# Kernel tuning notes

Hardware: AMD Instinct MI355X
Metric: run time of the kernel (lower is better)

Reference implementation:

```python
import jax, jax.numpy as jnp
import numpy as np

B = 128          # episodes
L = 512          # static pad length per episode (support or query)
LAMBDA_K_TAU = 0.1


def _masked_cov(x, mask, lengths):
    # x: [B, L, D]; mask: [B, L, 1]; lengths: [B] (float counts)
    x = x * mask
    mean = x.sum(axis=1) / lengths[:, None]                    # [B, D]
    c = (x - mean[:, None, :]) * mask                          # [B, L, D]
    cov = jnp.einsum('bld,ble->bde', c, c)                     # [B, D, D]
    return cov / (lengths - 1.0)[:, None, None]


def _calc_label_cov_inv(task_cov, label_cov):
    d = task_cov.shape[-1]
    eye = jnp.eye(d, dtype=task_cov.dtype)
    m = LAMBDA_K_TAU * label_cov + (1.0 - LAMBDA_K_TAU) * task_cov + 0.1 * eye
    return jnp.linalg.inv(m)


def _separate_qsl(graph_reprs, labels, is_query, batch_index):
    # Re-batch flat [N, D] into padded per-episode support/query tensors.
    N, D = graph_reprs.shape
    g = batch_index * 2 + is_query                             # group id
    perm = jnp.argsort(g)                                      # stable sort
    gs = g[perm]
    first = jnp.searchsorted(gs, gs, side='left')
    rank = jnp.arange(N) - first                               # index within group
    b = batch_index[perm]
    q = is_query[perm]
    row_s = jnp.where(q == 0, rank, L)                         # dummy row L for other kind
    row_q = jnp.where(q == 1, rank, L)
    xp = graph_reprs[perm]
    sup = jnp.zeros((B, L + 1, D), graph_reprs.dtype).at[b, row_s].set(xp)[:, :L]
    qry = jnp.zeros((B, L + 1, D), graph_reprs.dtype).at[b, row_q].set(xp)[:, :L]
    sup_lab = jnp.zeros((B, L + 1), labels.dtype).at[b, row_s].set(labels[perm])[:, :L]
    isq = is_query.astype(jnp.float32)
    sup_len = jnp.zeros((B,), jnp.float32).at[batch_index].add(1.0 - isq)
    qry_len = jnp.zeros((B,), jnp.float32).at[batch_index].add(isq)
    return sup, sup_lab, sup_len, qry, qry_len


def setup_inputs() -> dict:
    key = jax.random.key(0)
    k0, k1, k2, k3 = jax.random.split(key, 4)
    N, D = 49152, 512
    graph_reprs = jax.random.normal(k0, (N, D), jnp.float32)
    labels = jax.random.randint(k1, (N,), 0, 2)
    is_query = jax.random.randint(k2, (N,), 0, 2)
    batch_index = jnp.sort(jax.random.randint(k3, (N,), 0, B))
    log_scale = jnp.full((1,), np.log(1.0 / 16.0), jnp.float32)
    return {"graph_reprs": graph_reprs, "log_scale": log_scale,
            "labels": labels, "is_query": is_query, "batch_index": batch_index}


def reference(graph_reprs, log_scale, labels, is_query, batch_index):
    sup, sup_lab, sup_len, qry, qry_len = _separate_qsl(graph_reprs, labels, is_query, batch_index)
    f = jnp.float32
    support_mask = (jnp.arange(L)[None, :] < sup_len[:, None]).astype(f)[..., None]  # [B,L,1]
    mpos = (sup_lab == 1).astype(f)[..., None] * support_mask
    mneg = (sup_lab == 0).astype(f)[..., None] * support_mask

    pos_mean = (sup * mpos).sum(axis=1) / mpos.sum(axis=1)     # [B, D]
    neg_mean = (sup * mneg).sum(axis=1) / mneg.sum(axis=1)

    task_cov = _masked_cov(sup, support_mask, sup_len)
    pos_cnt = mpos.sum(axis=(1, 2))
    neg_cnt = mneg.sum(axis=(1, 2))
    # Masked covariance == cov of boolean-extracted, re-batched class subsets.
    pos_cov = _masked_cov(sup, mpos, pos_cnt)
    neg_cov = _masked_cov(sup, mneg, neg_cnt)

    pos_inv = _calc_label_cov_inv(task_cov, pos_cov)
    neg_inv = _calc_label_cov_inv(task_cov, neg_cov)

    query_mask = (jnp.arange(L)[None, :] < qry_len[:, None]).astype(f)  # [B, L]
    pos_diff = qry - pos_mean[:, None, :]
    neg_diff = qry - neg_mean[:, None, :]
    # Faithful to original einsum (sums inv over its second index):
    pos_maha = jnp.einsum('bik,bkx,bij->bi', pos_diff, pos_inv, pos_diff) * query_mask
    neg_maha = jnp.einsum('bik,bkx,bij->bi', neg_diff, neg_inv, neg_diff) * query_mask

    logits = jnp.stack([neg_maha, pos_maha], axis=-1)          # [B, L, 2]
    return logits * jnp.exp(log_scale)
```

## Files before the change

### kernel.cpp

```cpp
#include <hip/hip_runtime.h>
#include <cstdint>
#include <cstddef>

#define EPISODES 128
#define LPAD     512
#define DDIM     512
#define NS_CAP   320
#define GTILE    64
#define NPAIRS   15
#define CG_ITERS 14
#define GL_F4    10016
#define KCH      64
#define KSTR     72

typedef __attribute__((ext_vector_type(8))) __bf16 bf16x8;
typedef __attribute__((ext_vector_type(4))) float  floatx4;

__device__ __forceinline__ int lower_bound_dev(const int* __restrict__ a, int n, int key){
    int lo = 0, hi = n;
    while(lo < hi){
        int m = (lo + hi) >> 1;
        if(a[m] < key) lo = m + 1; else hi = m;
    }
    return lo;
}

__device__ __forceinline__ float4 f4add(float4 a, float4 b){
    return make_float4(a.x+b.x, a.y+b.y, a.z+b.z, a.w+b.w);
}
__device__ __forceinline__ float4 f4fma(float s, float4 a, float4 acc){
    return make_float4(acc.x + s*a.x, acc.y + s*a.y, acc.z + s*a.z, acc.w + s*a.w);
}
__device__ __forceinline__ float f4dot(float4 a, float4 b){
    return a.x*b.x + a.y*b.y + a.z*b.z + a.w*b.w;
}
__device__ __forceinline__ float f4sum(float4 a){ return (a.x+a.y)+(a.z+a.w); }

__device__ __forceinline__ unsigned short f2bf(float x){
    unsigned u = __float_as_uint(x);
    u += 0x7FFFu + ((u >> 16) & 1u);
    return (unsigned short)(u >> 16);
}
__device__ __forceinline__ float bf2f(unsigned short h){
    return __uint_as_float(((unsigned)h) << 16);
}

__device__ __forceinline__ float rdlanef(float v, int l){
    return __int_as_float(__builtin_amdgcn_readlane(__float_as_int(v), l));
}
__device__ __forceinline__ float dotb(float4 g, float4 u, int l){
    return g.x*rdlanef(u.x,l) + g.y*rdlanef(u.y,l)
         + g.z*rdlanef(u.z,l) + g.w*rdlanef(u.w,l);
}
__device__ __forceinline__ void gload_lds16(const float4* g, float4* l){
    __builtin_amdgcn_global_load_lds(
        (__attribute__((address_space(1))) void*)g,
        (__attribute__((address_space(3))) void*)l,
        16, 0, 0);
}

__global__ __launch_bounds__(256) void k_prep(
        const int* __restrict__ labels, const int* __restrict__ is_query,
        const int* __restrict__ bidx, const float* __restrict__ X, int N,
        int* __restrict__ sup_idx, int* __restrict__ qry_idx,
        int* __restrict__ sup_lab, int* __restrict__ counts,
        float* __restrict__ task_mean, float* __restrict__ pos_mean,
        float* __restrict__ neg_mean, float* __restrict__ row_sums2)
{
    const int bid  = blockIdx.x;
    const int b    = bid >> 1;
    const int h    = bid & 1;
    const int tid  = threadIdx.x;
    const int lane = tid & 63;
    const int wave = tid >> 6;

    __shared__ int s_start, s_end;
    __shared__ int wq[4];
    __shared__ int s_runq, s_npos;
    __shared__ int   sidx[NS_CAP];
    __shared__ float slabf[NS_CAP];
    __shared__ float4 pa[4][64];
    __shared__ float4 pp[4][64];

    if(tid == 0){
        s_start = lower_bound_dev(bidx, N, b);
        s_end   = lower_bound_dev(bidx, N, b + 1);
        s_runq  = 0;
        s_npos  = 0;
    }
    __syncthreads();
    const int start = s_start, end = s_end;

    for(int base = start; base < end; base += 256){
        int idx   = base + tid;
        bool valid = idx < end;
        int q   = valid ? is_query[idx] : 0;
        int lab = valid ? labels[idx]   : 0;
        unsigned long long m = __ballot(q == 1);
        if(lane == 0) wq[wave] = __popcll(m);
        __syncthreads();
        int woff = 0;
        for(int w = 0; w < wave; w++) woff += wq[w];
        int qbefore = __popcll(m & ((1ull << lane) - 1ull)) + woff;
        int runq0 = s_runq;
        int chunk_total = wq[0] + wq[1] + wq[2] + wq[3];
        if(valid){
            int pos_in_seg = idx - start;
            if(q){
                int qr = runq0 + qbefore;
                if(h == 0 && qr < LPAD) qry_idx[b * LPAD + qr] = idx;
            } else {
                int sr = pos_in_seg - runq0 - qbefore;
                if(sr < LPAD){
                    if(h == 0){
                        sup_idx[b * LPAD + sr] = idx;
                        sup_lab[b * LPAD + sr] = lab;
                    }
                    if(sr < NS_CAP){ sidx[sr] = idx; slabf[sr] = (float)lab; }
                    if(lab == 1) atomicAdd(&s_npos, 1);
                }
            }
        }
        __syncthreads();
        if(tid == 0) s_runq = runq0 + chunk_total;
        __syncthreads();
    }

    const int nq   = s_runq;
    const int ns   = (end - start) - nq;
    const int npos = s_npos;
    const int nneg = ns - npos;
    if(h == 0 && tid == 0){
        counts[b*4 + 0] = ns;
        counts[b*4 + 1] = nq;
        counts[b*4 + 2] = npos;
        counts[b*4 + 3] = nneg;
    }
    const int nsb = min(ns, NS_CAP);

    const float4* X4 = (const float4*)X;
    const int colg = h*64 + lane;
    float4 sa = make_float4(0.f,0.f,0.f,0.f);
    float4 sp = make_float4(0.f,0.f,0.f,0.f);
    int r = wave;
    for(; r + 12 < nsb; r += 16){
        int n0 = sidx[r], n1 = sidx[r+4], n2 = sidx[r+8], n3 = sidx[r+12];
        float l0 = slabf[r], l1 = slabf[r+4], l2 = slabf[r+8], l3 = slabf[r+12];
        float4 x0 = X4[(size_t)n0*128 + colg];
        float4 x1 = X4[(size_t)n1*128 + colg];
        float4 x2 = X4[(size_t)n2*128 + colg];
        float4 x3 = X4[(size_t)n3*128 + colg];
        sa = f4add(sa, f4add(f4add(x0,x1), f4add(x2,x3)));
        sp = f4fma(l0,x0, f4fma(l1,x1, f4fma(l2,x2, f4fma(l3,x3, sp))));
        float r0s = f4sum(x0), r1s = f4sum(x1), r2s = f4sum(x2), r3s = f4sum(x3);
        #pragma unroll
        for(int off = 32; off; off >>= 1){
            r0s += __shfl_xor(r0s, off); r1s += __shfl_xor(r1s, off);
            r2s += __shfl_xor(r2s, off); r3s += __shfl_xor(r3s, off);
        }
        if(lane == 0){
            row_sums2[(b*LPAD + r   )*2 + h] = r0s;
            row_sums2[(b*LPAD + r+4 )*2 + h] = r1s;
            row_sums2[(b*LPAD + r+8 )*2 + h] = r2s;
            row_sums2[(b*LPAD + r+12)*2 + h] = r3s;
        }
    }
    for(; r < nsb; r += 4){
        int n = sidx[r];
        float l = slabf[r];
        float4 x = X4[(size_t)n*128 + colg];
        sa = f4add(sa, x);
        sp = f4fma(l, x, sp);
        float rs = f4sum(x);
        #pragma unroll
        for(int off = 32; off; off >>= 1) rs += __shfl_xor(rs, off);
        if(lane == 0) row_sums2[(b*LPAD + r)*2 + h] = rs;
    }
    pa[wave][lane] = sa;
    pp[wave][lane] = sp;
    __syncthreads();
    if(tid < 64){
        float4 A = f4add(f4add(pa[0][tid],pa[1][tid]), f4add(pa[2][tid],pa[3][tid]));
        float4 P = f4add(f4add(pp[0][tid],pp[1][tid]), f4add(pp[2][tid],pp[3][tid]));
        float4 Nn = make_float4(A.x-P.x, A.y-P.y, A.z-P.z, A.w-P.w);
        float ia = 1.f/(float)ns, ip = 1.f/(float)npos, in = 1.f/(float)nneg;
        int c = b*128 + h*64 + tid;
        ((float4*)task_mean)[c] = make_float4(A.x*ia, A.y*ia, A.z*ia, A.w*ia);
        ((float4*)pos_mean )[c] = make_float4(P.x*ip, P.y*ip, P.z*ip, P.w*ip);
        ((float4*)neg_mean )[c] = make_float4(Nn.x*in, Nn.y*in, Nn.z*in, Nn.w*in);
    }
}

__global__ __launch_bounds__(256) void k_gram(
        const float* __restrict__ X, const int* __restrict__ sup_idx,
        const int* __restrict__ counts, float* __restrict__ G0)
{
    const int bid = blockIdx.x;
    const int b   = bid / NPAIRS;
    int tp = bid % NPAIRS;
    int ti = 0;
    while((ti+1)*(ti+2)/2 <= tp) ti++;
    const int tj  = tp - ti*(ti+1)/2;
    const int tid = threadIdx.x;
    const int lane = tid & 63;
    const int wave = tid >> 6;

    const int ns  = counts[b*4 + 0];
    const int nsc = min(ns, NS_CAP);
    if(ti * GTILE >= nsc) return;
    const bool diag = (ti == tj);

    __shared__ int ia[GTILE], ib[GTILE];
    __shared__ __align__(16) unsigned short SM[4 * GTILE * KSTR];
    unsigned short* SAh = SM;
    unsigned short* SAl = SM + GTILE*KSTR;
    unsigned short* SBh = SM + 2*GTILE*KSTR;
    unsigned short* SBl = SM + 3*GTILE*KSTR;

    if(tid < GTILE)        ia[tid]    = sup_idx[b*LPAD + min(ti*GTILE + tid,      nsc-1)];
    else if(tid < 2*GTILE) ib[tid-64] = sup_idx[b*LPAD + min(tj*GTILE + (tid-64), nsc-1)];

    const unsigned short* Bh = diag ? SAh : SBh;
    const unsigned short* Bl = diag ? SAl : SBl;

    const int ry = (wave >> 1) * 32;
    const int cx = (wave & 1) * 32;
    const int fr = lane & 15;
    const int fq = (lane >> 4) * 8;

    floatx4 acc[2][2];
    acc[0][0] = (floatx4){0.f,0.f,0.f,0.f};
    acc[0][1] = (floatx4){0.f,0.f,0.f,0.f};
    acc[1][0] = (floatx4){0.f,0.f,0.f,0.f};
    acc[1][1] = (floatx4){0.f,0.f,0.f,0.f};

    for(int k0 = 0; k0 < DDIM; k0 += KCH){
        __syncthreads();
        #pragma unroll
        for(int p = 0; p < 4; p++){
            int e = tid + p*256;
            int row = e >> 4, kq = e & 15;
            float4 xa = *(const float4*)(X + (size_t)ia[row]*DDIM + k0 + kq*4);
            ushort4 hh, ll;
            hh.x = f2bf(xa.x); ll.x = f2bf(xa.x - bf2f(hh.x));
            hh.y = f2bf(xa.y); ll.y = f2bf(xa.y - bf2f(hh.y));
            hh.z = f2bf(xa.z); ll.z = f2bf(xa.z - bf2f(hh.z));
            hh.w = f2bf(xa.w); ll.w = f2bf(xa.w - bf2f(hh.w));
            *(ushort4*)&SAh[row*KSTR + kq*4] = hh;
            *(ushort4*)&SAl[row*KSTR + kq*4] = ll;
            if(!diag){
                float4 xb = *(const float4*)(X + (size_t)ib[row]*DDIM + k0 + kq*4);
                ushort4 h2, l2;
                h2.x = f2bf(xb.x); l2.x = f2bf(xb.x - bf2f(h2.x));
                h2.y = f2bf(xb.y); l2.y = f2bf(xb.y - bf2f(h2.y));
                h2.z = f2bf(xb.z); l2.z = f2bf(xb.z - bf2f(h2.z));
                h2.w = f2bf(xb.w); l2.w = f2bf(xb.w - bf2f(h2.w));
                *(ushort4*)&SBh[row*KSTR + kq*4] = h2;
                *(ushort4*)&SBl[row*KSTR + kq*4] = l2;
            }
        }
        __syncthreads();
        #pragma unroll
        for(int ks = 0; ks < KCH; ks += 32){
            bf16x8 ah0 = *(const bf16x8*)&SAh[(ry     + fr)*KSTR + ks + fq];
            bf16x8 ah1 = *(const bf16x8*)&SAh[(ry + 16 + fr)*KSTR + ks + fq];
            bf16x8 al0 = *(const bf16x8*)&SAl[(ry     + fr)*KSTR + ks + fq];
            bf16x8 al1 = *(const bf16x8*)&SAl[(ry + 16 + fr)*KSTR + ks + fq];
            bf16x8 bh0 = *(const bf16x8*)&Bh[(cx     + fr)*KSTR + ks + fq];
            bf16x8 bh1 = *(const bf16x8*)&Bh[(cx + 16 + fr)*KSTR + ks + fq];
            bf16x8 bl0 = *(const bf16x8*)&Bl[(cx     + fr)*KSTR + ks + fq];
            bf16x8 bl1 = *(const bf16x8*)&Bl[(cx + 16 + fr)*KSTR + ks + fq];
            acc[0][0] = __builtin_amdgcn_mfma_f32_16x16x32_bf16(ah0, bh0, acc[0][0], 0,0,0);
            acc[0][1] = __builtin_amdgcn_mfma_f32_16x16x32_bf16(ah0, bh1, acc[0][1], 0,0,0);
            acc[1][0] = __builtin_amdgcn_mfma_f32_16x16x32_bf16(ah1, bh0, acc[1][0], 0,0,0);
            acc[1][1] = __builtin_amdgcn_mfma_f32_16x16x32_bf16(ah1, bh1, acc[1][1], 0,0,0);
            acc[0][0] = __builtin_amdgcn_mfma_f32_16x16x32_bf16(ah0, bl0, acc[0][0], 0,0,0);
            acc[0][1] = __builtin_amdgcn_mfma_f32_16x16x32_bf16(ah0, bl1, acc[0][1], 0,0,0);
            acc[1][0] = __builtin_amdgcn_mfma_f32_16x16x32_bf16(ah1, bl0, acc[1][0], 0,0,0);
            acc[1][1] = __builtin_amdgcn_mfma_f32_16x16x32_bf16(ah1, bl1, acc[1][1], 0,0,0);
            acc[0][0] = __builtin_amdgcn_mfma_f32_16x16x32_bf16(al0, bh0, acc[0][0], 0,0,0);
            acc[0][1] = __builtin_amdgcn_mfma_f32_16x16x32_bf16(al0, bh1, acc[0][1], 0,0,0);
            acc[1][0] = __builtin_amdgcn_mfma_f32_16x16x32_bf16(al1, bh0, acc[1][0], 0,0,0);
            acc[1][1] = __builtin_amdgcn_mfma_f32_16x16x32_bf16(al1, bh1, acc[1][1], 0,0,0);
        }
    }

    float4* Gf4 = (float4*)(G0 + (size_t)b * NS_CAP * NS_CAP);
    const int q = lane >> 4, j = lane & 15;
    #pragma unroll
    for(int sy = 0; sy < 2; sy++)
        #pragma unroll
        for(int sx = 0; sx < 2; sx++){
            int cq = ((ti*GTILE + ry + sy*16) >> 2) + q;
            int t  = tj*GTILE + cx + sx*16 + j;
            Gf4[(size_t)cq * NS_CAP + t] =
                make_float4(acc[sy][sx].x, acc[sy][sx].y, acc[sy][sx].z, acc[sy][sx].w);
        }

    if(!diag){
        __syncthreads();
        float* Tb = (float*)SM;
        #pragma unroll
        for(int sy = 0; sy < 2; sy++)
            #pragma unroll
            for(int sx = 0; sx < 2; sx++){
                int r0 = ry + sy*16 + 4*q;
                int c  = cx + sx*16 + j;
                Tb[(r0+0)*68 + c] = acc[sy][sx].x;
                Tb[(r0+1)*68 + c] = acc[sy][sx].y;
                Tb[(r0+2)*68 + c] = acc[sy][sx].z;
                Tb[(r0+3)*68 + c] = acc[sy][sx].w;
            }
        __syncthreads();
        for(int e = tid; e < 16*GTILE; e += 256){
            int cc = e >> 6;
            int r  = e & 63;
            float4 v = *(const float4*)&Tb[r*68 + 4*cc];
            Gf4[(size_t)(tj*16 + cc) * NS_CAP + ti*GTILE + r] = v;
        }
    }
}

extern __shared__ float4 gl4[];

__global__ __launch_bounds__(512, 2) void k_cgc(
        const float* __restrict__ X, const float* __restrict__ G0,
        const int* __restrict__ sup_idx, const int* __restrict__ sup_lab,
        const int* __restrict__ counts, const float* __restrict__ row_sums2,
        float* __restrict__ vout)
{
    const int bid  = blockIdx.x;
    const int sys  = ((bid & 7) << 5) | (bid >> 3);
    const int b    = sys >> 1;
    const int cls  = sys & 1;
    const int tid  = threadIdx.x;
    const int lane = tid & 63;
    const int wave = tid >> 6;

    __shared__ __align__(16) float u[NS_CAP];
    __shared__ int   idx_l[NS_CAP];
    __shared__ float P[64];

    const int ns   = counts[b*4 + 0];
    const int nsc  = min(ns, NS_CAP);
    const int ncls = cls ? counts[b*4 + 2] : counts[b*4 + 3];
    const float c_task = 0.9f / (float)(ns - 1);
    const float c_cls  = 0.1f / (float)(ncls - 1);
    const float inv_ns = 1.f / (float)ns;
    const float inv_nc = 1.f / (float)ncls;
    const float4* G4 = (const float4*)(G0 + (size_t)b * NS_CAP * NS_CAP);
    const float4* u4 = (const float4*)u;
    const int nf4 = (nsc + 3) >> 2;
    const int c4l = min(nf4, GL_F4 / nsc);

    const bool mth = tid < NS_CAP;
    const bool own = tid < nsc;
    float mfl = 0.f, sraw = 0.f;
    if(own){
        mfl  = (sup_lab[b*LPAD + tid] == cls) ? 1.f : 0.f;
        float2 rs = ((const float2*)row_sums2)[b*LPAD + tid];
        sraw = rs.x + rs.y;
    }
    for(int s = tid; s < nsc; s += 512) idx_l[s] = sup_idx[b*LPAD + s];
    if(tid < 64) P[tid] = 0.f;

    {
        const int nchunk = (nsc + 63) >> 6;
        for(int ch = 0; ch < nchunk; ch++){
            const int t = (ch << 6) + lane;
            const bool act = t < nsc;
            const float4* gsrc = G4 + t;
            float4*       ldst = gl4 + t;
            for(int c4 = wave; c4 < c4l; c4 += 8){
                if(act) gload_lds16(gsrc + (size_t)c4 * NS_CAP, ldst + c4 * nsc);
            }
        }
    }
    __syncthreads();

    auto bundle = [&](float v0, float v1, float v2, float v3, float v4,
                      float* S){
        #pragma unroll
        for(int off = 32; off; off >>= 1){
            v0 += __shfl_xor(v0, off); v1 += __shfl_xor(v1, off);
            v2 += __shfl_xor(v2, off); v3 += __shfl_xor(v3, off);
            v4 += __shfl_xor(v4, off);
        }
        if(lane == 0){
            P[wave*8 + 0] = v0; P[wave*8 + 1] = v1; P[wave*8 + 2] = v2;
            P[wave*8 + 3] = v3; P[wave*8 + 4] = v4;
        }
        __syncthreads();
        float pv = P[lane];
        pv += __shfl_xor(pv, 8);
        pv += __shfl_xor(pv, 16);
        pv += __shfl_xor(pv, 32);
        S[0] = __shfl(pv, 0); S[1] = __shfl(pv, 1); S[2] = __shfl(pv, 2);
        S[3] = __shfl(pv, 3); S[4] = __shfl(pv, 4);
    };

    const bool fastu = (nf4 <= 64);

    auto matvec = [&]() -> float {
        float s0 = 0.f, s1 = 0.f, s2 = 0.f, s3 = 0.f;
        if(fastu){
            if((wave << 6) < nsc){
                float4 ubc = u4[lane < nf4 ? lane : 0];
                asm volatile("" : "+v"(ubc.x), "+v"(ubc.y), "+v"(ubc.z), "+v"(ubc.w));
                const int row = own ? tid : (nsc - 1);
                const float4* gq = gl4 + row;
                int c4 = 0;
                for(; c4 + 8 <= c4l; c4 += 8){
                    float4 g0 = gq[(c4+0)*nsc], g1 = gq[(c4+1)*nsc];
                    float4 g2 = gq[(c4+2)*nsc], g3 = gq[(c4+3)*nsc];
                    float4 g4_ = gq[(c4+4)*nsc], g5 = gq[(c4+5)*nsc];
                    float4 g6 = gq[(c4+6)*nsc], g7 = gq[(c4+7)*nsc];
                    s0 += dotb(g0, ubc, c4+0); s1 += dotb(g1, ubc, c4+1);
                    s2 += dotb(g2, ubc, c4+2); s3 += dotb(g3, ubc, c4+3);
                    s0 += dotb(g4_, ubc, c4+4); s1 += dotb(g5, ubc, c4+5);
                    s2 += dotb(g6, ubc, c4+6); s3 += dotb(g7, ubc, c4+7);
                }
                for(; c4 < c4l; c4++) s0 += dotb(gq[c4*nsc], ubc, c4);
                for(; c4 + 4 <= nf4; c4 += 4){
                    float4 h0 = G4[(size_t)(c4+0)*NS_CAP + row];
                    float4 h1 = G4[(size_t)(c4+1)*NS_CAP + row];
                    float4 h2 = G4[(size_t)(c4+2)*NS_CAP + row];
                    float4 h3 = G4[(size_t)(c4+3)*NS_CAP + row];
                    s0 += dotb(h0, ubc, c4+0); s1 += dotb(h1, ubc, c4+1);
                    s2 += dotb(h2, ubc, c4+2); s3 += dotb(h3, ubc, c4+3);
                }
                for(; c4 < nf4; c4++)
                    s0 += dotb(G4[(size_t)c4*NS_CAP + row], ubc, c4);
            }
        } else {
            if(own){
                const float4* gq = gl4 + tid;
                int c4 = 0;
                for(; c4 + 8 <= c4l; c4 += 8){
                    float4 g0 = gq[(c4+0)*nsc], g1 = gq[(c4+1)*nsc];
                    float4 g2 = gq[(c4+2)*nsc], g3 = gq[(c4+3)*nsc];
                    float4 g4_ = gq[(c4+4)*nsc], g5 = gq[(c4+5)*nsc];
                    float4 g6 = gq[(c4+6)*nsc], g7 = gq[(c4+7)*nsc];
                    s0 += f4dot(g0, u4[c4+0]); s1 += f4dot(g1, u4[c4+1]);
                    s2 += f4dot(g2, u4[c4+2]); s3 += f4dot(g3, u4[c4+3]);
                    s0 += f4dot(g4_, u4[c4+4]); s1 += f4dot(g5, u4[c4+5]);
                    s2 += f4dot(g6, u4[c4+6]); s3 += f4dot(g7, u4[c4+7]);
                }
                for(; c4 < c4l; c4++) s0 += f4dot(gq[c4*nsc], u4[c4]);
                for(; c4 + 8 <= nf4; c4 += 8){
                    float4 g[8];
                    #pragma unroll
                    for(int jj = 0; jj < 8; jj++) g[jj] = G4[(size_t)(c4+jj)*NS_CAP + tid];
                    #pragma unroll
                    for(int jj = 0; jj < 8; jj++){
                        float d = f4dot(g[jj], u4[c4+jj]);
                        if((jj & 3) == 0) s0 += d; else if((jj & 3) == 1) s1 += d;
                        else if((jj & 3) == 2) s2 += d; else s3 += d;
                    }
                }
                for(; c4 < nf4; c4++) s0 += f4dot(G4[(size_t)c4*NS_CAP + tid], u4[c4]);
            }
        }
        float t = (s0 + s1) + (s2 + s3);
        return own ? t : 0.f;
    };

    float S[5];
    bundle(sraw, mfl * sraw, 0.f, 0.f, 0.f, S);
    float A0 = S[0] * inv_ns, A1 = S[1] * inv_nc;
    float cr = own ? -10.f * (c_task*(sraw - A0) + mfl*c_cls*(sraw - A1)) : 0.f;
    if(mth) u[tid] = cr;
    __syncthreads();
    float tr = matvec();

    float cp = 0.f, cq = 0.f, tq = 0.f, cx = 0.f;
    float gamma_old = 1.f, alpha_old = 1.f;
    bool first = true;

    for(int it = 0; it < CG_ITERS; ++it){
        bundle(tr, mfl*tr, tr*tr, mfl*tr*tr, tr*cr, S);
        A0 = S[0] * inv_ns; A1 = S[1] * inv_nc;
        float gamma = S[4];
        float delta = 0.1f*gamma + c_task*(S[2] - S[0]*A0)
                                 + c_cls *(S[3] - S[1]*A1);
        float beta  = first ? 0.f : gamma / gamma_old;
        float denom = first ? delta : (delta - beta * gamma / alpha_old);
        float alpha = (gamma < 1e-30f) ? 0.f : gamma / denom;
        float ur = own ? (c_task*(tr - A0) + mfl*c_cls*(tr - A1)) : 0.f;
        float cw = 0.1f*cr + ur;
        cp = cr + beta * cp;
        cq = cw + beta * cq;
        cx += alpha * cp;
        if(it == CG_ITERS - 1 || gamma < 1e-26f) break;
        if(mth) u[tid] = ur;
        __syncthreads();
        float gv = matvec();
        float tw = 0.1f*tr + gv;
        tq = tw + beta * tq;
        cr -= alpha * cq;
        tr -= alpha * tq;
        gamma_old = gamma; alpha_old = alpha; first = false;
    }

    __syncthreads();
    if(mth) u[tid] = own ? cx : 0.f;
    __syncthreads();
    const float4* X4 = (const float4*)X;
    const int f4c = tid & 127;
    const int rg  = tid >> 7;
    float4 acc = make_float4(0.f,0.f,0.f,0.f);
    int s = rg;
    for(; s + 28 < nsc; s += 32){
        int n0 = idx_l[s],    n1 = idx_l[s+4],  n2 = idx_l[s+8],  n3 = idx_l[s+12];
        int n4 = idx_l[s+16], n5 = idx_l[s+20], n6 = idx_l[s+24], n7 = idx_l[s+28];
        float w0 = u[s],    w1 = u[s+4],  w2 = u[s+8],  w3 = u[s+12];
        float w4 = u[s+16], w5 = u[s+20], w6 = u[s+24], w7 = u[s+28];
        float4 x0 = X4[(size_t)n0*128 + f4c];
        float4 x1 = X4[(size_t)n1*128 + f4c];
        float4 x2 = X4[(size_t)n2*128 + f4c];
        float4 x3 = X4[(size_t)n3*128 + f4c];
        float4 x4 = X4[(size_t)n4*128 + f4c];
        float4 x5 = X4[(size_t)n5*128 + f4c];
        float4 x6 = X4[(size_t)n6*128 + f4c];
        float4 x7 = X4[(size_t)n7*128 + f4c];
        acc = f4fma(w0,x0, f4fma(w1,x1, f4fma(w2,x2, f4fma(w3,x3, acc))));
        acc = f4fma(w4,x4, f4fma(w5,x5, f4fma(w6,x6, f4fma(w7,x7, acc))));
    }
    for(; s < nsc; s += 4)
        acc = f4fma(u[s], X4[(size_t)idx_l[s]*128 + f4c], acc);
    gl4[rg*128 + f4c] = acc;
    __syncthreads();
    if(tid < 128){
        float4 v = f4add(f4add(gl4[tid], gl4[128+tid]),
                         f4add(gl4[256+tid], gl4[384+tid]));
        v.x += 10.f; v.y += 10.f; v.z += 10.f; v.w += 10.f;
        ((float4*)vout)[(size_t)sys * 128 + tid] = v;
    }
}

__global__ __launch_bounds__(256) void k_out(
        const float* __restrict__ X,
        const int* __restrict__ qry_idx, const int* __restrict__ counts,
        const float* __restrict__ pos_mean, const float* __restrict__ neg_mean,
        const float* __restrict__ vsol, const float* __restrict__ log_scale,
        float* __restrict__ out)
{
    const int bid  = blockIdx.x;
    const int b    = bid >> 1;
    const int h    = bid & 1;
    const int tid  = threadIdx.x;
    const int lane = tid & 63;
    const int wave = tid >> 6;

    __shared__ __align__(16) float vpos[DDIM];
    __shared__ __align__(16) float vneg[DDIM];
    __shared__ float red4[4][4];
    __shared__ float sc[4];

    const int nq  = counts[b*4 + 1];
    const int nqc = min(nq, LPAD);
    const float scale = expf(log_scale[0]);

    float pm0 = pos_mean[b*DDIM + tid], pm1 = pos_mean[b*DDIM + tid + 256];
    float nm0 = neg_mean[b*DDIM + tid], nm1 = neg_mean[b*DDIM + tid + 256];
    float vp0 = vsol[(size_t)(b*2 + 1) * DDIM + tid];
    float vp1 = vsol[(size_t)(b*2 + 1) * DDIM + tid + 256];
    float vn0 = vsol[(size_t)(b*2 + 0) * DDIM + tid];
    float vn1 = vsol[(size_t)(b*2 + 0) * DDIM + tid + 256];
    vpos[tid] = vp0; vpos[tid + 256] = vp1;
    vneg[tid] = vn0; vneg[tid + 256] = vn1;

    float smp = pm0 + pm1;
    float smn = nm0 + nm1;
    float mvp = pm0 * vp0 + pm1 * vp1;
    float mvn = nm0 * vn0 + nm1 * vn1;
    #pragma unroll
    for(int off = 32; off; off >>= 1){
        smp += __shfl_xor(smp, off);
        smn += __shfl_xor(smn, off);
        mvp += __shfl_xor(mvp, off);
        mvn += __shfl_xor(mvn, off);
    }
    if(lane == 0){
        red4[wave][0] = smp; red4[wave][1] = smn;
        red4[wave][2] = mvp; red4[wave][3] = mvn;
    }
    __syncthreads();
    if(tid < 4) sc[tid] = red4[0][tid] + red4[1][tid] + red4[2][tid] + red4[3][tid];
    __syncthreads();

    const float4* vp4 = (const float4*)vpos;
    const float4* vn4 = (const float4*)vneg;
    const float4 vpa = vp4[lane], vpb = vp4[lane + 64];
    const float4 vna = vn4[lane], vnb = vn4[lane + 64];
    for(int r = wave + 4*h; r < nqc; r += 16){
        int r2 = r + 8;
        bool has2 = r2 < nqc;
        int n  = qry_idx[b * LPAD + r];
        int n2 = qry_idx[b * LPAD + (has2 ? r2 : r)];
        const float4* xr = (const float4*)(X + (size_t)n  * DDIM);
        const float4* yr = (const float4*)(X + (size_t)n2 * DDIM);
        float4 x0 = xr[lane], x1 = xr[lane + 64];
        float4 y0 = yr[lane], y1 = yr[lane + 64];
        float tp = f4dot(x0, vpa) + f4dot(x1, vpb);
        float tn = f4dot(x0, vna) + f4dot(x1, vnb);
        float sx = f4sum(x0) + f4sum(x1);
        float tp2 = f4dot(y0, vpa) + f4dot(y1, vpb);
        float tn2 = f4dot(y0, vna) + f4dot(y1, vnb);
        float sx2 = f4sum(y0) + f4sum(y1);
        #pragma unroll
        for(int off = 32; off; off >>= 1){
            tp  += __shfl_xor(tp,  off);
            tn  += __shfl_xor(tn,  off);
            sx  += __shfl_xor(sx,  off);
            tp2 += __shfl_xor(tp2, off);
            tn2 += __shfl_xor(tn2, off);
            sx2 += __shfl_xor(sx2, off);
        }
        if(lane == 0){
            float mp = (tp - sc[2]) * (sx - sc[0]);
            float mn = (tn - sc[3]) * (sx - sc[1]);
            ((float2*)out)[(size_t)b * LPAD + r] = make_float2(mn * scale, mp * scale);
            if(has2){
                float mp2 = (tp2 - sc[2]) * (sx2 - sc[0]);
                float mn2 = (tn2 - sc[3]) * (sx2 - sc[1]);
                ((float2*)out)[(size_t)b * LPAD + r2] = make_float2(mn2 * scale, mp2 * scale);
            }
        }
    }
    const int lo = max(nqc, h * 256), hi = (h + 1) * 256;
    for(int r = lo + tid; r < hi; r += 256)
        ((float2*)out)[(size_t)b * LPAD + r] = make_float2(0.f, 0.f);
}

extern "C" void kernel_launch(void* const* d_in, const int* in_sizes, int n_in,
                              void* d_out, int out_size, void* d_ws, size_t ws_size,
                              hipStream_t stream)
{
    const float* X         = (const float*)d_in[0];
    const float* log_scale = (const float*)d_in[1];
    const int*   labels    = (const int*)d_in[2];
    const int*   is_query  = (const int*)d_in[3];
    const int*   bidx      = (const int*)d_in[4];
    const int N = in_sizes[2];

    char* ws = (char*)d_ws;
    auto alloc = [&](size_t bytes) -> char* {
        char* p = ws;
        ws += (bytes + 255) & ~(size_t)255;
        return p;
    };
    int*   sup_idx   = (int*)  alloc((size_t)EPISODES * LPAD * sizeof(int));
    int*   qry_idx   = (int*)  alloc((size_t)EPISODES * LPAD * sizeof(int));
    int*   sup_lab   = (int*)  alloc((size_t)EPISODES * LPAD * sizeof(int));
    int*   counts    = (int*)  alloc((size_t)EPISODES * 4 * sizeof(int));
    float* task_mean = (float*)alloc((size_t)EPISODES * DDIM * sizeof(float));
    float* pos_mean  = (float*)alloc((size_t)EPISODES * DDIM * sizeof(float));
    float* neg_mean  = (float*)alloc((size_t)EPISODES * DDIM * sizeof(float));
    float* vsol      = (float*)alloc((size_t)EPISODES * 2 * DDIM * sizeof(float));
    float* row_sums2 = (float*)alloc((size_t)EPISODES * LPAD * 2 * sizeof(float));
    float* G0        = (float*)alloc((size_t)EPISODES * NS_CAP * NS_CAP * sizeof(float));
    (void)ws_size;
    (void)task_mean;

    k_prep<<<EPISODES*2, 256, 0, stream>>>(labels, is_query, bidx, X, N,
                                           sup_idx, qry_idx, sup_lab, counts,
                                           task_mean, pos_mean, neg_mean, row_sums2);
    k_gram<<<EPISODES * NPAIRS, 256, 0, stream>>>(X, sup_idx, counts, G0);
    k_cgc<<<EPISODES * 2, 512, GL_F4 * sizeof(float4), stream>>>(
                                            X, G0, sup_idx, sup_lab, counts,
                                            row_sums2, vsol);
    k_out<<<EPISODES*2, 256, 0, stream>>>(X, qry_idx, counts, pos_mean, neg_mean,
                                          vsol, log_scale, (float*)d_out);
}
```

Baseline: 307.2 us.

## Enlarge Gram tiles to 96 and split CG matvec columns across two thread halves

The Gram kernel now uses 96x96 tiles with a 3x3 MFMA fragment grid per wave, cutting the number of tile pairs from 15 to 10 and reusing each loaded fragment more often. Because tiles no longer divide the 320 cap evenly, stores are bounds-guarded. In the CG kernel the fast matvec path splits the column range between the two 256-thread halves and combines the partial sums through shared memory with an extra barrier. The shared-memory budget is shrunk slightly to fit the exchange buffer. The costs are higher register pressure from nine accumulators, wasted work on partial edge tiles, and one more sync per matvec.

```diff
diff --git a/kernel.cpp b/kernel.cpp
--- a/kernel.cpp
+++ b/kernel.cpp
@@ -6,10 +6,10 @@
 #define LPAD     512
 #define DDIM     512
 #define NS_CAP   320
-#define GTILE    64
-#define NPAIRS   15
+#define GTILE    96
+#define NPAIRS   10
 #define CG_ITERS 14
-#define GL_F4    10016
+#define GL_F4    9984
 #define KCH      64
 #define KSTR     72
 
@@ -217,27 +217,28 @@
     unsigned short* SBh = SM + 2*GTILE*KSTR;
     unsigned short* SBl = SM + 3*GTILE*KSTR;
 
-    if(tid < GTILE)        ia[tid]    = sup_idx[b*LPAD + min(ti*GTILE + tid,      nsc-1)];
-    else if(tid < 2*GTILE) ib[tid-64] = sup_idx[b*LPAD + min(tj*GTILE + (tid-64), nsc-1)];
+    if(tid < GTILE)        ia[tid]     = sup_idx[b*LPAD + min(ti*GTILE + tid,       nsc-1)];
+    else if(tid < 2*GTILE) ib[tid-96]  = sup_idx[b*LPAD + min(tj*GTILE + (tid-96),  nsc-1)];
 
     const unsigned short* Bh = diag ? SAh : SBh;
     const unsigned short* Bl = diag ? SAl : SBl;
 
-    const int ry = (wave >> 1) * 32;
-    const int cx = (wave & 1) * 32;
+    const int ry = (wave >> 1) * 48;
+    const int cx = (wave & 1) * 48;
     const int fr = lane & 15;
     const int fq = (lane >> 4) * 8;
 
-    floatx4 acc[2][2];
-    acc[0][0] = (floatx4){0.f,0.f,0.f,0.f};
-    acc[0][1] = (floatx4){0.f,0.f,0.f,0.f};
-    acc[1][0] = (floatx4){0.f,0.f,0.f,0.f};
-    acc[1][1] = (floatx4){0.f,0.f,0.f,0.f};
+    floatx4 acc[3][3];
+    #pragma unroll
+    for(int m = 0; m < 3; m++)
+        #pragma unroll
+        for(int n = 0; n < 3; n++)
+            acc[m][n] = (floatx4){0.f,0.f,0.f,0.f};
 
     for(int k0 = 0; k0 < DDIM; k0 += KCH){
         __syncthreads();
         #pragma unroll
-        for(int p = 0; p < 4; p++){
+        for(int p = 0; p < 6; p++){
             int e = tid + p*256;
             int row = e >> 4, kq = e & 15;
             float4 xa = *(const float4*)(X + (size_t)ia[row]*DDIM + k0 + kq*4);
@@ -262,61 +263,62 @@
         __syncthreads();
         #pragma unroll
         for(int ks = 0; ks < KCH; ks += 32){
-            bf16x8 ah0 = *(const bf16x8*)&SAh[(ry     + fr)*KSTR + ks + fq];
-            bf16x8 ah1 = *(const bf16x8*)&SAh[(ry + 16 + fr)*KSTR + ks + fq];
-            bf16x8 al0 = *(const bf16x8*)&SAl[(ry     + fr)*KSTR + ks + fq];
-            bf16x8 al1 = *(const bf16x8*)&SAl[(ry + 16 + fr)*KSTR + ks + fq];
-            bf16x8 bh0 = *(const bf16x8*)&Bh[(cx     + fr)*KSTR + ks + fq];
-            bf16x8 bh1 = *(const bf16x8*)&Bh[(cx + 16 + fr)*KSTR + ks + fq];
-            bf16x8 bl0 = *(const bf16x8*)&Bl[(cx     + fr)*KSTR + ks + fq];
-            bf16x8 bl1 = *(const bf16x8*)&Bl[(cx + 16 + fr)*KSTR + ks + fq];
-            acc[0][0] = __builtin_amdgcn_mfma_f32_16x16x32_bf16(ah0, bh0, acc[0][0], 0,0,0);
-            acc[0][1] = __builtin_amdgcn_mfma_f32_16x16x32_bf16(ah0, bh1, acc[0][1], 0,0,0);
-            acc[1][0] = __builtin_amdgcn_mfma_f32_16x16x32_bf16(ah1, bh0, acc[1][0], 0,0,0);
-            acc[1][1] = __builtin_amdgcn_mfma_f32_16x16x32_bf16(ah1, bh1, acc[1][1], 0,0,0);
-            acc[0][0] = __builtin_amdgcn_mfma_f32_16x16x32_bf16(ah0, bl0, acc[0][0], 0,0,0);
-            acc[0][1] = __builtin_amdgcn_mfma_f32_16x16x32_bf16(ah0, bl1, acc[0][1], 0,0,0);
-            acc[1][0] = __builtin_amdgcn_mfma_f32_16x16x32_bf16(ah1, bl0, acc[1][0], 0,0,0);
-            acc[1][1] = __builtin_amdgcn_mfma_f32_16x16x32_bf16(ah1, bl1, acc[1][1], 0,0,0);
-            acc[0][0] = __builtin_amdgcn_mfma_f32_16x16x32_bf16(al0, bh0, acc[0][0], 0,0,0);
-            acc[0][1] = __builtin_amdgcn_mfma_f32_16x16x32_bf16(al0, bh1, acc[0][1], 0,0,0);
-            acc[1][0] = __builtin_amdgcn_mfma_f32_16x16x32_bf16(al1, bh0, acc[1][0], 0,0,0);
-            acc[1][1] = __builtin_amdgcn_mfma_f32_16x16x32_bf16(al1, bh1, acc[1][1], 0,0,0);
+            bf16x8 ah[3], al[3], bh[3], bl[3];
+            #pragma unroll
+            for(int m = 0; m < 3; m++){
+                ah[m] = *(const bf16x8*)&SAh[(ry + 16*m + fr)*KSTR + ks + fq];
+                al[m] = *(const bf16x8*)&SAl[(ry + 16*m + fr)*KSTR + ks + fq];
+                bh[m] = *(const bf16x8*)&Bh [(cx + 16*m + fr)*KSTR + ks + fq];
+                bl[m] = *(const bf16x8*)&Bl [(cx + 16*m + fr)*KSTR + ks + fq];
+            }
+            #pragma unroll
+            for(int m = 0; m < 3; m++)
+                #pragma unroll
+                for(int n = 0; n < 3; n++){
+                    acc[m][n] = __builtin_amdgcn_mfma_f32_16x16x32_bf16(ah[m], bh[n], acc[m][n], 0,0,0);
+                    acc[m][n] = __builtin_amdgcn_mfma_f32_16x16x32_bf16(ah[m], bl[n], acc[m][n], 0,0,0);
+                    acc[m][n] = __builtin_amdgcn_mfma_f32_16x16x32_bf16(al[m], bh[n], acc[m][n], 0,0,0);
+                }
         }
     }
 
     float4* Gf4 = (float4*)(G0 + (size_t)b * NS_CAP * NS_CAP);
     const int q = lane >> 4, j = lane & 15;
     #pragma unroll
-    for(int sy = 0; sy < 2; sy++)
-        #pragma unroll
-        for(int sx = 0; sx < 2; sx++){
+    for(int sy = 0; sy < 3; sy++)
+        #pragma unroll
+        for(int sx = 0; sx < 3; sx++){
             int cq = ((ti*GTILE + ry + sy*16) >> 2) + q;
             int t  = tj*GTILE + cx + sx*16 + j;
-            Gf4[(size_t)cq * NS_CAP + t] =
-                make_float4(acc[sy][sx].x, acc[sy][sx].y, acc[sy][sx].z, acc[sy][sx].w);
+            if(cq < (NS_CAP >> 2) && t < NS_CAP)
+                Gf4[(size_t)cq * NS_CAP + t] =
+                    make_float4(acc[sy][sx].x, acc[sy][sx].y, acc[sy][sx].z, acc[sy][sx].w);
         }
 
     if(!diag){
         __syncthreads();
         float* Tb = (float*)SM;
         #pragma unroll
-        for(int sy = 0; sy < 2; sy++)
+        for(int sy = 0; sy < 3; sy++)
             #pragma unroll
-            for(int sx = 0; sx < 2; sx++){
+            for(int sx = 0; sx < 3; sx++){
                 int r0 = ry + sy*16 + 4*q;
                 int c  = cx + sx*16 + j;
-                Tb[(r0+0)*68 + c] = acc[sy][sx].x;
-                Tb[(r0+1)*68 + c] = acc[sy][sx].y;
-                Tb[(r0+2)*68 + c] = acc[sy][sx].z;
-                Tb[(r0+3)*68 + c] = acc[sy][sx].w;
-            }
-        __syncthreads();
-        for(int e = tid; e < 16*GTILE; e += 256){
-            int cc = e >> 6;
-            int r  = e & 63;
-            float4 v = *(const float4*)&Tb[r*68 + 4*cc];
-            Gf4[(size_t)(tj*16 + cc) * NS_CAP + ti*GTILE + r] = v;
+                Tb[(r0+0)*100 + c] = acc[sy][sx].x;
+                Tb[(r0+1)*100 + c] = acc[sy][sx].y;
+                Tb[(r0+2)*100 + c] = acc[sy][sx].z;
+                Tb[(r0+3)*100 + c] = acc[sy][sx].w;
+            }
+        __syncthreads();
+        for(int e = tid; e < 24*GTILE; e += 256){
+            int cc = e / GTILE;
+            int r  = e - cc*GTILE;
+            int gq2 = tj*24 + cc;
+            int t2  = ti*GTILE + r;
+            if(gq2 < (NS_CAP >> 2) && t2 < NS_CAP){
+                float4 v = *(const float4*)&Tb[r*100 + 4*cc];
+                Gf4[(size_t)gq2 * NS_CAP + t2] = v;
+            }
         }
     }
 }
@@ -336,10 +338,13 @@
     const int tid  = threadIdx.x;
     const int lane = tid & 63;
     const int wave = tid >> 6;
+    const int half = tid >> 8;
+    const int hrow = tid & 255;
 
     __shared__ __align__(16) float u[NS_CAP];
     __shared__ int   idx_l[NS_CAP];
     __shared__ float P[64];
+    __shared__ float exch[256];
 
     const int ns   = counts[b*4 + 0];
     const int nsc  = min(ns, NS_CAP);
@@ -352,6 +357,7 @@
     const float4* u4 = (const float4*)u;
     const int nf4 = (nsc + 3) >> 2;
     const int c4l = min(nf4, GL_F4 / nsc);
+    const int c4m = min(nf4, ((nf4 >> 1) + 3) & ~3);
 
     const bool mth = tid < NS_CAP;
     const bool own = tid < nsc;
@@ -402,15 +408,20 @@
     const bool fastu = (nf4 <= 64);
 
     auto matvec = [&]() -> float {
-        float s0 = 0.f, s1 = 0.f, s2 = 0.f, s3 = 0.f;
         if(fastu){
-            if((wave << 6) < nsc){
+            float p = 0.f;
+            if(((wave & 3) << 6) < nsc){
                 float4 ubc = u4[lane < nf4 ? lane : 0];
                 asm volatile("" : "+v"(ubc.x), "+v"(ubc.y), "+v"(ubc.z), "+v"(ubc.w));
-                const int row = own ? tid : (nsc - 1);
+                const bool ownr = hrow < nsc;
+                const int row = ownr ? hrow : (nsc - 1);
                 const float4* gq = gl4 + row;
-                int c4 = 0;
-                for(; c4 + 8 <= c4l; c4 += 8){
+                float s0 = 0.f, s1 = 0.f, s2 = 0.f, s3 = 0.f;
+                const int lo = half ? c4m : 0;
+                const int hi = half ? nf4 : c4m;
+                const int lim = min(hi, c4l);
+                int c4 = lo;
+                for(; c4 + 8 <= lim; c4 += 8){
                     float4 g0 = gq[(c4+0)*nsc], g1 = gq[(c4+1)*nsc];
                     float4 g2 = gq[(c4+2)*nsc], g3 = gq[(c4+3)*nsc];
                     float4 g4_ = gq[(c4+4)*nsc], g5 = gq[(c4+5)*nsc];
@@ -420,8 +431,8 @@
                     s0 += dotb(g4_, ubc, c4+4); s1 += dotb(g5, ubc, c4+5);
                     s2 += dotb(g6, ubc, c4+6); s3 += dotb(g7, ubc, c4+7);
                 }
-                for(; c4 < c4l; c4++) s0 += dotb(gq[c4*nsc], ubc, c4);
-                for(; c4 + 4 <= nf4; c4 += 4){
+                for(; c4 < lim; c4++) s0 += dotb(gq[c4*nsc], ubc, c4);
+                for(; c4 + 4 <= hi; c4 += 4){
                     float4 h0 = G4[(size_t)(c4+0)*NS_CAP + row];
                     float4 h1 = G4[(size_t)(c4+1)*NS_CAP + row];
                     float4 h2 = G4[(size_t)(c4+2)*NS_CAP + row];
@@ -429,10 +440,16 @@
                     s0 += dotb(h0, ubc, c4+0); s1 += dotb(h1, ubc, c4+1);
                     s2 += dotb(h2, ubc, c4+2); s3 += dotb(h3, ubc, c4+3);
                 }
-                for(; c4 < nf4; c4++)
+                for(; c4 < hi; c4++)
                     s0 += dotb(G4[(size_t)c4*NS_CAP + row], ubc, c4);
-            }
+                p = ownr ? ((s0 + s1) + (s2 + s3)) : 0.f;
+            }
+            if(half) exch[hrow] = p;
+            __syncthreads();
+            float t = (half == 0 && own) ? (p + exch[hrow]) : 0.f;
+            return t;
         } else {
+            float s0 = 0.f, s1 = 0.f, s2 = 0.f, s3 = 0.f;
             if(own){
                 const float4* gq = gl4 + tid;
                 int c4 = 0;
@@ -460,9 +477,9 @@
                 }
                 for(; c4 < nf4; c4++) s0 += f4dot(G4[(size_t)c4*NS_CAP + tid], u4[c4]);
             }
-        }
-        float t = (s0 + s1) + (s2 + s3);
-        return own ? t : 0.f;
+            float t = (s0 + s1) + (s2 + s3);
+            return own ? t : 0.f;
+        }
     };
 
     float S[5];
```

Measured after the change: 340.7 us. 10.9% more time.

## Precompute bf16 hi/lo support rows in prep and split CG matvec across halves

Applied to the files above, without the earlier changes.

k_prep now writes split bf16 hi/lo copies of the gathered support rows into a packed per-episode workspace, zero-padded to a 64-row boundary. k_gram then loads these tiles straight into XOR-swizzled LDS with global_load_lds, so it no longer does gathered fp32 loads and per-tile conversion repeated across tile pairs. In k_cgc's fast matvec path, both 256-thread halves of the block now take half of the columns each and combine partial sums through shared memory, with a slight LDS budget cut. The cost is extra global writes and workspace for the bf16 copy, plus an added barrier in every matvec.

```diff
diff --git a/kernel.cpp b/kernel.cpp
--- a/kernel.cpp
+++ b/kernel.cpp
@@ -9,9 +9,9 @@
 #define GTILE    64
 #define NPAIRS   15
 #define CG_ITERS 14
-#define GL_F4    10016
+#define GL_F4    9984
 #define KCH      64
-#define KSTR     72
+#define XBF_ROW  1024
 
 typedef __attribute__((ext_vector_type(8))) __bf16 bf16x8;
 typedef __attribute__((ext_vector_type(4))) float  floatx4;
@@ -44,6 +44,12 @@
 __device__ __forceinline__ float bf2f(unsigned short h){
     return __uint_as_float(((unsigned)h) << 16);
 }
+__device__ __forceinline__ void cvt_hilo(float4 x, ushort4& hh, ushort4& ll){
+    hh.x = f2bf(x.x); ll.x = f2bf(x.x - bf2f(hh.x));
+    hh.y = f2bf(x.y); ll.y = f2bf(x.y - bf2f(hh.y));
+    hh.z = f2bf(x.z); ll.z = f2bf(x.z - bf2f(hh.z));
+    hh.w = f2bf(x.w); ll.w = f2bf(x.w - bf2f(hh.w));
+}
 
 __device__ __forceinline__ float rdlanef(float v, int l){
     return __int_as_float(__builtin_amdgcn_readlane(__float_as_int(v), l));
@@ -52,9 +58,9 @@
     return g.x*rdlanef(u.x,l) + g.y*rdlanef(u.y,l)
          + g.z*rdlanef(u.z,l) + g.w*rdlanef(u.w,l);
 }
-__device__ __forceinline__ void gload_lds16(const float4* g, float4* l){
+__device__ __forceinline__ void gload_lds16(const void* g, void* l){
     __builtin_amdgcn_global_load_lds(
-        (__attribute__((address_space(1))) void*)g,
+        (const __attribute__((address_space(1))) void*)g,
         (__attribute__((address_space(3))) void*)l,
         16, 0, 0);
 }
@@ -65,7 +71,8 @@
         int* __restrict__ sup_idx, int* __restrict__ qry_idx,
         int* __restrict__ sup_lab, int* __restrict__ counts,
         float* __restrict__ task_mean, float* __restrict__ pos_mean,
-        float* __restrict__ neg_mean, float* __restrict__ row_sums2)
+        float* __restrict__ neg_mean, float* __restrict__ row_sums2,
+        unsigned short* __restrict__ Xbf)
 {
     const int bid  = blockIdx.x;
     const int b    = bid >> 1;
@@ -152,6 +159,22 @@
         float4 x3 = X4[(size_t)n3*128 + colg];
         sa = f4add(sa, f4add(f4add(x0,x1), f4add(x2,x3)));
         sp = f4fma(l0,x0, f4fma(l1,x1, f4fma(l2,x2, f4fma(l3,x3, sp))));
+        {
+            ushort4 hh, ll;
+            size_t rb;
+            rb = ((size_t)(b*NS_CAP + r   ) << 10);
+            cvt_hilo(x0, hh, ll);
+            *(ushort4*)&Xbf[rb + colg*4] = hh;  *(ushort4*)&Xbf[rb + 512 + colg*4] = ll;
+            rb = ((size_t)(b*NS_CAP + r+4 ) << 10);
+            cvt_hilo(x1, hh, ll);
+            *(ushort4*)&Xbf[rb + colg*4] = hh;  *(ushort4*)&Xbf[rb + 512 + colg*4] = ll;
+            rb = ((size_t)(b*NS_CAP + r+8 ) << 10);
+            cvt_hilo(x2, hh, ll);
+            *(ushort4*)&Xbf[rb + colg*4] = hh;  *(ushort4*)&Xbf[rb + 512 + colg*4] = ll;
+            rb = ((size_t)(b*NS_CAP + r+12) << 10);
+            cvt_hilo(x3, hh, ll);
+            *(ushort4*)&Xbf[rb + colg*4] = hh;  *(ushort4*)&Xbf[rb + 512 + colg*4] = ll;
+        }
         float r0s = f4sum(x0), r1s = f4sum(x1), r2s = f4sum(x2), r3s = f4sum(x3);
         #pragma unroll
         for(int off = 32; off; off >>= 1){
@@ -171,10 +194,25 @@
         float4 x = X4[(size_t)n*128 + colg];
         sa = f4add(sa, x);
         sp = f4fma(l, x, sp);
+        {
+            ushort4 hh, ll;
+            size_t rb = ((size_t)(b*NS_CAP + r) << 10);
+            cvt_hilo(x, hh, ll);
+            *(ushort4*)&Xbf[rb + colg*4] = hh;  *(ushort4*)&Xbf[rb + 512 + colg*4] = ll;
+        }
         float rs = f4sum(x);
         #pragma unroll
         for(int off = 32; off; off >>= 1) rs += __shfl_xor(rs, off);
         if(lane == 0) row_sums2[(b*LPAD + r)*2 + h] = rs;
+    }
+    {
+        const int padf = min((nsb + 63) & ~63, NS_CAP);
+        ushort4 z; z.x = z.y = z.z = z.w = 0;
+        for(int rz = nsb + wave; rz < padf; rz += 4){
+            size_t rb = ((size_t)(b*NS_CAP + rz) << 10);
+            *(ushort4*)&Xbf[rb + colg*4] = z;
+            *(ushort4*)&Xbf[rb + 512 + colg*4] = z;
+        }
     }
     pa[wave][lane] = sa;
     pp[wave][lane] = sp;
@@ -192,7 +230,7 @@
 }
 
 __global__ __launch_bounds__(256) void k_gram(
-        const float* __restrict__ X, const int* __restrict__ sup_idx,
+        const unsigned short* __restrict__ Xbf,
         const int* __restrict__ counts, float* __restrict__ G0)
 {
     const int bid = blockIdx.x;
@@ -210,23 +248,18 @@
     if(ti * GTILE >= nsc) return;
     const bool diag = (ti == tj);
 
-    __shared__ int ia[GTILE], ib[GTILE];
-    __shared__ __align__(16) unsigned short SM[4 * GTILE * KSTR];
-    unsigned short* SAh = SM;
-    unsigned short* SAl = SM + GTILE*KSTR;
-    unsigned short* SBh = SM + 2*GTILE*KSTR;
-    unsigned short* SBl = SM + 3*GTILE*KSTR;
-
-    if(tid < GTILE)        ia[tid]    = sup_idx[b*LPAD + min(ti*GTILE + tid,      nsc-1)];
-    else if(tid < 2*GTILE) ib[tid-64] = sup_idx[b*LPAD + min(tj*GTILE + (tid-64), nsc-1)];
-
-    const unsigned short* Bh = diag ? SAh : SBh;
-    const unsigned short* Bl = diag ? SAl : SBl;
-
+    __shared__ __align__(16) unsigned short SM[4 * GTILE * 64];
+    unsigned short* const SAh = SM;
+    unsigned short* const SAl = SM + 4096;
+    const unsigned short* Bh = diag ? SAh : (SM + 8192);
+    const unsigned short* Bl = diag ? SAl : (SM + 12288);
+
+    const int r8  = lane >> 3;
+    const int blk = lane & 7;
+    const int fr = lane & 15;
+    const int fq = (lane >> 4) * 8;
     const int ry = (wave >> 1) * 32;
     const int cx = (wave & 1) * 32;
-    const int fr = lane & 15;
-    const int fq = (lane >> 4) * 8;
 
     floatx4 acc[2][2];
     acc[0][0] = (floatx4){0.f,0.f,0.f,0.f};
@@ -234,42 +267,44 @@
     acc[1][0] = (floatx4){0.f,0.f,0.f,0.f};
     acc[1][1] = (floatx4){0.f,0.f,0.f,0.f};
 
+    const int xr = blk ^ r8;
     for(int k0 = 0; k0 < DDIM; k0 += KCH){
         __syncthreads();
         #pragma unroll
-        for(int p = 0; p < 4; p++){
-            int e = tid + p*256;
-            int row = e >> 4, kq = e & 15;
-            float4 xa = *(const float4*)(X + (size_t)ia[row]*DDIM + k0 + kq*4);
-            ushort4 hh, ll;
-            hh.x = f2bf(xa.x); ll.x = f2bf(xa.x - bf2f(hh.x));
-            hh.y = f2bf(xa.y); ll.y = f2bf(xa.y - bf2f(hh.y));
-            hh.z = f2bf(xa.z); ll.z = f2bf(xa.z - bf2f(hh.z));
-            hh.w = f2bf(xa.w); ll.w = f2bf(xa.w - bf2f(hh.w));
-            *(ushort4*)&SAh[row*KSTR + kq*4] = hh;
-            *(ushort4*)&SAl[row*KSTR + kq*4] = ll;
-            if(!diag){
-                float4 xb = *(const float4*)(X + (size_t)ib[row]*DDIM + k0 + kq*4);
-                ushort4 h2, l2;
-                h2.x = f2bf(xb.x); l2.x = f2bf(xb.x - bf2f(h2.x));
-                h2.y = f2bf(xb.y); l2.y = f2bf(xb.y - bf2f(h2.y));
-                h2.z = f2bf(xb.z); l2.z = f2bf(xb.z - bf2f(h2.z));
-                h2.w = f2bf(xb.w); l2.w = f2bf(xb.w - bf2f(h2.w));
-                *(ushort4*)&SBh[row*KSTR + kq*4] = h2;
-                *(ushort4*)&SBl[row*KSTR + kq*4] = l2;
+        for(int i = 0; i < 4; i++){
+            int e  = wave*4 + i;
+            int pl = e >> 3, g = e & 7;
+            int row = g*8 + r8;
+            const unsigned short* src = Xbf
+                + ((size_t)(b*NS_CAP + ti*GTILE + row) << 10)
+                + pl*512 + k0 + (xr << 3);
+            gload_lds16(src, SM + pl*4096 + row*64 + blk*8);
+        }
+        if(!diag){
+            #pragma unroll
+            for(int i = 0; i < 4; i++){
+                int e  = wave*4 + i;
+                int pl = e >> 3, g = e & 7;
+                int row = g*8 + r8;
+                const unsigned short* src = Xbf
+                    + ((size_t)(b*NS_CAP + tj*GTILE + row) << 10)
+                    + pl*512 + k0 + (xr << 3);
+                gload_lds16(src, SM + 8192 + pl*4096 + row*64 + blk*8);
             }
         }
         __syncthreads();
         #pragma unroll
         for(int ks = 0; ks < KCH; ks += 32){
-            bf16x8 ah0 = *(const bf16x8*)&SAh[(ry     + fr)*KSTR + ks + fq];
-            bf16x8 ah1 = *(const bf16x8*)&SAh[(ry + 16 + fr)*KSTR + ks + fq];
-            bf16x8 al0 = *(const bf16x8*)&SAl[(ry     + fr)*KSTR + ks + fq];
-            bf16x8 al1 = *(const bf16x8*)&SAl[(ry + 16 + fr)*KSTR + ks + fq];
-            bf16x8 bh0 = *(const bf16x8*)&Bh[(cx     + fr)*KSTR + ks + fq];
-            bf16x8 bh1 = *(const bf16x8*)&Bh[(cx + 16 + fr)*KSTR + ks + fq];
-            bf16x8 bl0 = *(const bf16x8*)&Bl[(cx     + fr)*KSTR + ks + fq];
-            bf16x8 bl1 = *(const bf16x8*)&Bl[(cx + 16 + fr)*KSTR + ks + fq];
+            const int j  = (ks + fq) >> 3;
+            const int jx = (j ^ (fr & 7)) << 3;
+            bf16x8 ah0 = *(const bf16x8*)&SAh[(ry      + fr)*64 + jx];
+            bf16x8 ah1 = *(const bf16x8*)&SAh[(ry + 16 + fr)*64 + jx];
+            bf16x8 al0 = *(const bf16x8*)&SAl[(ry      + fr)*64 + jx];
+            bf16x8 al1 = *(const bf16x8*)&SAl[(ry + 16 + fr)*64 + jx];
+            bf16x8 bh0 = *(const bf16x8*)&Bh [(cx      + fr)*64 + jx];
+            bf16x8 bh1 = *(const bf16x8*)&Bh [(cx + 16 + fr)*64 + jx];
+            bf16x8 bl0 = *(const bf16x8*)&Bl [(cx      + fr)*64 + jx];
+            bf16x8 bl1 = *(const bf16x8*)&Bl [(cx + 16 + fr)*64 + jx];
             acc[0][0] = __builtin_amdgcn_mfma_f32_16x16x32_bf16(ah0, bh0, acc[0][0], 0,0,0);
             acc[0][1] = __builtin_amdgcn_mfma_f32_16x16x32_bf16(ah0, bh1, acc[0][1], 0,0,0);
             acc[1][0] = __builtin_amdgcn_mfma_f32_16x16x32_bf16(ah1, bh0, acc[1][0], 0,0,0);
@@ -336,10 +371,13 @@
     const int tid  = threadIdx.x;
     const int lane = tid & 63;
     const int wave = tid >> 6;
+    const int half = tid >> 8;
+    const int hrow = tid & 255;
 
     __shared__ __align__(16) float u[NS_CAP];
     __shared__ int   idx_l[NS_CAP];
     __shared__ float P[64];
+    __shared__ float exch[256];
 
     const int ns   = counts[b*4 + 0];
     const int nsc  = min(ns, NS_CAP);
@@ -352,6 +390,7 @@
     const float4* u4 = (const float4*)u;
     const int nf4 = (nsc + 3) >> 2;
     const int c4l = min(nf4, GL_F4 / nsc);
+    const int c4m = min(nf4, ((nf4 >> 1) + 3) & ~3);
 
     const bool mth = tid < NS_CAP;
     const bool own = tid < nsc;
@@ -402,15 +441,20 @@
     const bool fastu = (nf4 <= 64);
 
     auto matvec = [&]() -> float {
-        float s0 = 0.f, s1 = 0.f, s2 = 0.f, s3 = 0.f;
         if(fastu){
-            if((wave << 6) < nsc){
+            float p = 0.f;
+            if(((wave & 3) << 6) < nsc){
                 float4 ubc = u4[lane < nf4 ? lane : 0];
                 asm volatile("" : "+v"(ubc.x), "+v"(ubc.y), "+v"(ubc.z), "+v"(ubc.w));
-                const int row = own ? tid : (nsc - 1);
+                const bool ownr = hrow < nsc;
+                const int row = ownr ? hrow : (nsc - 1);
                 const float4* gq = gl4 + row;
-                int c4 = 0;
-                for(; c4 + 8 <= c4l; c4 += 8){
+                float s0 = 0.f, s1 = 0.f, s2 = 0.f, s3 = 0.f;
+                const int lo = half ? c4m : 0;
+                const int hi = half ? nf4 : c4m;
+                const int lim = min(hi, c4l);
+                int c4 = lo;
+                for(; c4 + 8 <= lim; c4 += 8){
                     float4 g0 = gq[(c4+0)*nsc], g1 = gq[(c4+1)*nsc];
                     float4 g2 = gq[(c4+2)*nsc], g3 = gq[(c4+3)*nsc];
                     float4 g4_ = gq[(c4+4)*nsc], g5 = gq[(c4+5)*nsc];
@@ -420,8 +464,8 @@
                     s0 += dotb(g4_, ubc, c4+4); s1 += dotb(g5, ubc, c4+5);
                     s2 += dotb(g6, ubc, c4+6); s3 += dotb(g7, ubc, c4+7);
                 }
-                for(; c4 < c4l; c4++) s0 += dotb(gq[c4*nsc], ubc, c4);
-                for(; c4 + 4 <= nf4; c4 += 4){
+                for(; c4 < lim; c4++) s0 += dotb(gq[c4*nsc], ubc, c4);
+                for(; c4 + 4 <= hi; c4 += 4){
                     float4 h0 = G4[(size_t)(c4+0)*NS_CAP + row];
                     float4 h1 = G4[(size_t)(c4+1)*NS_CAP + row];
                     float4 h2 = G4[(size_t)(c4+2)*NS_CAP + row];
@@ -429,10 +473,16 @@
                     s0 += dotb(h0, ubc, c4+0); s1 += dotb(h1, ubc, c4+1);
                     s2 += dotb(h2, ubc, c4+2); s3 += dotb(h3, ubc, c4+3);
                 }
-                for(; c4 < nf4; c4++)
+                for(; c4 < hi; c4++)
                     s0 += dotb(G4[(size_t)c4*NS_CAP + row], ubc, c4);
+                p = ownr ? ((s0 + s1) + (s2 + s3)) : 0.f;
             }
+            if(half) exch[hrow] = p;
+            __syncthreads();
+            float t = (half == 0 && own) ? (p + exch[hrow]) : 0.f;
+            return t;
         } else {
+            float s0 = 0.f, s1 = 0.f, s2 = 0.f, s3 = 0.f;
             if(own){
                 const float4* gq = gl4 + tid;
                 int c4 = 0;
@@ -460,9 +510,9 @@
                 }
                 for(; c4 < nf4; c4++) s0 += f4dot(G4[(size_t)c4*NS_CAP + tid], u4[c4]);
             }
-        }
-        float t = (s0 + s1) + (s2 + s3);
-        return own ? t : 0.f;
+            float t = (s0 + s1) + (s2 + s3);
+            return own ? t : 0.f;
+        }
     };
 
     float S[5];
@@ -660,13 +710,16 @@
     float* vsol      = (float*)alloc((size_t)EPISODES * 2 * DDIM * sizeof(float));
     float* row_sums2 = (float*)alloc((size_t)EPISODES * LPAD * 2 * sizeof(float));
     float* G0        = (float*)alloc((size_t)EPISODES * NS_CAP * NS_CAP * sizeof(float));
+    unsigned short* Xbf = (unsigned short*)alloc(
+                          (size_t)EPISODES * NS_CAP * XBF_ROW * sizeof(unsigned short));
     (void)ws_size;
     (void)task_mean;
 
     k_prep<<<EPISODES*2, 256, 0, stream>>>(labels, is_query, bidx, X, N,
                                            sup_idx, qry_idx, sup_lab, counts,
-                                           task_mean, pos_mean, neg_mean, row_sums2);
-    k_gram<<<EPISODES * NPAIRS, 256, 0, stream>>>(X, sup_idx, counts, G0);
+                                           task_mean, pos_mean, neg_mean, row_sums2,
+                                           Xbf);
+    k_gram<<<EPISODES * NPAIRS, 256, 0, stream>>>(Xbf, counts, G0);
     k_cgc<<<EPISODES * 2, 512, GL_F4 * sizeof(float4), stream>>>(
                                             X, G0, sup_idx, sup_lab, counts,
                                             row_sums2, vsol);
```

After: 297.1 us. 3.3% less time.
